# Kernel tuning notes

Measured on AMD Instinct MI355X. Metric: run time of the kernel, lower is better.

## Reference

```python
import jax, jax.numpy as jnp
import numpy as np

SNUM = 8           # number of select-PUF stages
PUF_LEN = 64       # arbiter PUF length -> phi dim = PUF_LEN + 1
BATCH = 262144     # number of challenge-response pairs
D = 2 ** SNUM      # 256 combinations


def _make_kron_tables():
    """Replicates the W/B kron construction from combineMPUF.__init__.
    Returns Wmat, Bmat of shape [SNUM, D]; row i is W[i]/B[i] (originally [1, D])."""
    tmpX = np.array([[1], [1]])
    Ws, Bs = [], []
    for i in range(SNUM):
        w = np.array([[-1], [1]])
        b = np.array([[1], [0]])
        for _ in range(i + 1, SNUM):
            w = np.kron(tmpX, w)
            b = np.kron(tmpX, b)
        for _ in range(i):
            w = np.kron(w, tmpX)
            b = np.kron(b, tmpX)
        Ws.append(w.T[0])
        Bs.append(b.T[0])
    return (jnp.asarray(np.stack(Ws), jnp.float32),
            jnp.asarray(np.stack(Bs), jnp.float32))


def setup_inputs() -> dict:
    key = jax.random.key(0)
    k_phi, k_ws, k_bs, k_wd, k_bd = jax.random.split(key, 5)
    F = PUF_LEN + 1
    scale = 1.0 / np.sqrt(F)  # ~ torch Linear init scale
    phi = jax.random.normal(k_phi, (BATCH, F), dtype=jnp.float32)
    W_S = jax.random.uniform(k_ws, (SNUM, F), jnp.float32, -scale, scale)
    b_S = jax.random.uniform(k_bs, (SNUM,), jnp.float32, -scale, scale)
    W_D = jax.random.uniform(k_wd, (D, F), jnp.float32, -scale, scale)
    b_D = jax.random.uniform(k_bd, (D,), jnp.float32, -scale, scale)
    Wmat, Bmat = _make_kron_tables()
    return {"phi": phi, "W_S": W_S, "b_S": b_S, "W_D": W_D, "b_D": b_D,
            "Wmat": Wmat, "Bmat": Bmat}


def reference(phi, W_S, b_S, W_D, b_D, Wmat, Bmat):
    # phi: [B, F]; W_S: [SNUM, F]; W_D: [D, F]; Wmat/Bmat: [SNUM, D]
    Sdelta = phi @ W_S.T + b_S            # [B, SNUM]
    Ddelta = phi @ W_D.T + b_D            # [B, D]
    Souts = jax.nn.sigmoid(Sdelta)        # [B, SNUM]
    Douts = jax.nn.sigmoid(Ddelta)        # [B, D]
    # sigmoid-gated outer-product chain: M = prod_i (s_i * w_i + b_i)
    M = jnp.ones_like(Douts)
    for i in range(SNUM):                 # small fixed structural loop
        M = M * (Souts[:, i:i + 1] * Wmat[i] + Bmat[i])
    ans = jnp.sum(Douts * M * 0.99999, axis=-1, keepdims=True)  # [B, 1]
    reliability_output = jnp.abs(Sdelta)  # [B, SNUM]
    return ans, reliability_output
```

## Files before the change

### kernel.cpp

```cpp
#include <hip/hip_runtime.h>

typedef float  f32x4  __attribute__((ext_vector_type(4)));
typedef float  f32x4a __attribute__((ext_vector_type(4), aligned(4)));
typedef __bf16 bf16x8 __attribute__((ext_vector_type(8)));
typedef short  short8 __attribute__((ext_vector_type(8)));

#define F      65
#define NTT    17
#define KS3    3
#define RPB    256
#define NCHUNK (NTT*KS3*64)
#define NEGL2E -1.4426950408889634f

__device__ __forceinline__ float fast_sigmoid(float x) {
  float e = __builtin_amdgcn_exp2f(NEGL2E * x);
  return __builtin_amdgcn_rcpf(1.0f + e);
}
__device__ __forceinline__ float sig_prescaled(float a) {
  return __builtin_amdgcn_rcpf(1.0f + __builtin_amdgcn_exp2f(a));
}
template<int CTRL>
__device__ __forceinline__ float dpp_mov(float v) {
  return __builtin_bit_cast(float,
    __builtin_amdgcn_update_dpp(0, __builtin_bit_cast(int, v), CTRL, 0xF, 0xF, true));
}
__device__ __forceinline__ float reduce16(float v) {
  v += dpp_mov<0xB1>(v);
  v += dpp_mov<0x4E>(v);
  v += dpp_mov<0x141>(v);
  v += dpp_mov<0x140>(v);
  return v;
}

__global__ void prep_w(const float* __restrict__ W_S, const float* __restrict__ b_S,
                       const float* __restrict__ W_D, const float* __restrict__ b_D,
                       unsigned short* __restrict__ wsb) {
  int b = blockIdx.x;
  int t = b / 3, s = b % 3;
  int l = threadIdx.x;
  int c = l & 15, q = l >> 4;
  short8 out;
#pragma unroll
  for (int j = 0; j < 8; ++j) {
    int k = 32 * s + 8 * q + j;
    float v = 0.0f;
    if (t < 16) {
      int n = 16 * t + c;
      if (k < F)       v = NEGL2E * W_D[n * F + k];
      else if (k == F) v = NEGL2E * b_D[n];
    } else if (c < 8) {
      if (k < F)       v = W_S[c * F + k];
      else if (k == F) v = b_S[c];
    }
    unsigned int u = __builtin_bit_cast(unsigned int, v);
    u += 0x7FFFu + ((u >> 16) & 1u);
    out[j] = (short)(u >> 16);
  }
  reinterpret_cast<short8*>(wsb)[b * 64 + l] = out;
}

__launch_bounds__(512, 4)
__global__ void mpuf_main(const float* __restrict__ phi,
                          const unsigned short* __restrict__ wsb,
                          float* __restrict__ out_ans,
                          float* __restrict__ out_rel) {
  __shared__ short8 ldsB[NCHUNK];
  __shared__ float  soutv[RPB][12];
  __shared__ float  mtT[16][260];

  const int tid  = threadIdx.x;
  const int wave = tid >> 6;
  const int l    = tid & 63;
  const int c    = l & 15;
  const int q    = l >> 4;
  const int wrow = wave * 32;
  const int R0b  = wrow + q * 4;
  const int brow = blockIdx.x * RPB;

  float* relbuf = &mtT[0][0];

  const float* prow0 = phi + (size_t)(brow + wrow + c) * F;
  const float* prow1 = prow0 + (size_t)16 * F;

  f32x4a f40[4], f41[4];
#pragma unroll
  for (int s = 0; s < 2; ++s) {
    f40[2 * s]     = *reinterpret_cast<const f32x4a*>(prow0 + 32 * s + 8 * q);
    f40[2 * s + 1] = *reinterpret_cast<const f32x4a*>(prow0 + 32 * s + 8 * q + 4);
    f41[2 * s]     = *reinterpret_cast<const f32x4a*>(prow1 + 32 * s + 8 * q);
    f41[2 * s + 1] = *reinterpret_cast<const f32x4a*>(prow1 + 32 * s + 8 * q + 4);
  }
  const float a640 = prow0[64];
  const float a641 = prow1[64];

  const short8* wsv = reinterpret_cast<const short8*>(wsb);
#pragma unroll
  for (int i = 0; i < 7; ++i) {
    int idx = tid + i * 512;
    if (idx < NCHUNK) ldsB[idx] = wsv[idx];
  }

  bf16x8 af0[3], af1[3];
#pragma unroll
  for (int s = 0; s < 2; ++s) {
    bf16x8 v0, v1;
#pragma unroll
    for (int j = 0; j < 4; ++j) {
      v0[j]     = (__bf16)f40[s * 2][j];
      v0[j + 4] = (__bf16)f40[s * 2 + 1][j];
      v1[j]     = (__bf16)f41[s * 2][j];
      v1[j + 4] = (__bf16)f41[s * 2 + 1][j];
    }
    af0[s] = v0; af1[s] = v1;
  }
  {
    bf16x8 v0 = {}, v1 = {};
    if (q == 0) {
      v0[0] = (__bf16)a640; v0[1] = (__bf16)1.0f;
      v1[0] = (__bf16)a641; v1[1] = (__bf16)1.0f;
    }
    af0[2] = v0; af1[2] = v1;
  }

  __syncthreads();

  f32x4 aS0 = {}, aS1 = {};
#pragma unroll
  for (int s = 0; s < KS3; ++s) {
    bf16x8 b = __builtin_bit_cast(bf16x8, ldsB[(16 * KS3 + s) * 64 + l]);
    aS0 = __builtin_amdgcn_mfma_f32_16x16x32_bf16(af0[s], b, aS0, 0, 0, 0);
    aS1 = __builtin_amdgcn_mfma_f32_16x16x32_bf16(af1[s], b, aS1, 0, 0, 0);
  }

  short8 bnxt[3];
#pragma unroll
  for (int s = 0; s < 3; ++s) bnxt[s] = ldsB[s * 64 + l];

  if (c < 8) {
#pragma unroll
    for (int r = 0; r < 4; ++r) {
      const int R0 = R0b + r, R1 = R0 + 16;
      relbuf[R0 * 8 + c] = fabsf(aS0[r]);
      relbuf[R1 * 8 + c] = fabsf(aS1[r]);
      soutv[R0][c] = fast_sigmoid(aS0[r]);
      soutv[R1][c] = fast_sigmoid(aS1[r]);
    }
  }

  {
    const int row = l >> 1, half = l & 1;
    f32x4 v = *reinterpret_cast<const f32x4*>(&relbuf[(wrow + row) * 8 + half * 4]);
    *reinterpret_cast<f32x4*>(
        &out_rel[(size_t)(brow + wrow + row) * 8 + half * 4]) = v;
  }

  __syncthreads();

  float Ml0[4], Ml1[4];
#pragma unroll
  for (int rr = 0; rr < 8; ++rr) {
    const int R = wrow + (rr & 4) * 4 + q * 4 + (rr & 3);
    f32x4 s03 = *reinterpret_cast<const f32x4*>(&soutv[R][0]);
    f32x4 s47 = *reinterpret_cast<const f32x4*>(&soutv[R][4]);
    float m = 0.99999f;
    m *= (c & 1) ? s03[0] : 1.0f - s03[0];
    m *= (c & 2) ? s03[1] : 1.0f - s03[1];
    m *= (c & 4) ? s03[2] : 1.0f - s03[2];
    m *= (c & 8) ? s03[3] : 1.0f - s03[3];
    if (rr < 4) Ml0[rr & 3] = m; else Ml1[rr & 3] = m;
    float mt = (c & 1) ? s47[0] : 1.0f - s47[0];
    mt *= (c & 2) ? s47[1] : 1.0f - s47[1];
    mt *= (c & 4) ? s47[2] : 1.0f - s47[2];
    mt *= (c & 8) ? s47[3] : 1.0f - s47[3];
    mtT[c][R] = mt;
  }

  float ans0[4] = {0, 0, 0, 0}, ans1[4] = {0, 0, 0, 0};

#pragma unroll 1
  for (int t = 0; t < 16; ++t) {
    short8 bt[3];
#pragma unroll
    for (int s = 0; s < 3; ++s) bt[s] = bnxt[s];
    const int tn = (t < 15) ? t + 1 : 15;
#pragma unroll
    for (int s = 0; s < 3; ++s)
      bnxt[s] = ldsB[(tn * KS3 + s) * 64 + l];
    f32x4 w0 = *reinterpret_cast<const f32x4*>(&mtT[t][R0b]);
    f32x4 w1 = *reinterpret_cast<const f32x4*>(&mtT[t][R0b + 16]);
    f32x4 A0 = {}, A1 = {};
#pragma unroll
    for (int s = 0; s < KS3; ++s) {
      bf16x8 b = __builtin_bit_cast(bf16x8, bt[s]);
      A0 = __builtin_amdgcn_mfma_f32_16x16x32_bf16(af0[s], b, A0, 0, 0, 0);
      A1 = __builtin_amdgcn_mfma_f32_16x16x32_bf16(af1[s], b, A1, 0, 0, 0);
    }
#pragma unroll
    for (int r = 0; r < 4; ++r) {
      ans0[r] = fmaf(sig_prescaled(A0[r]), w0[r], ans0[r]);
      ans1[r] = fmaf(sig_prescaled(A1[r]), w1[r], ans1[r]);
    }
  }

  f32x4 o0, o1;
#pragma unroll
  for (int r = 0; r < 4; ++r) {
    o0[r] = reduce16(Ml0[r] * ans0[r]);
    o1[r] = reduce16(Ml1[r] * ans1[r]);
  }
  if (c == 0) {
    *reinterpret_cast<f32x4*>(&out_ans[brow + wrow + q * 4])      = o0;
    *reinterpret_cast<f32x4*>(&out_ans[brow + wrow + 16 + q * 4]) = o1;
  }
}

extern "C" void kernel_launch(void* const* d_in, const int* in_sizes, int n_in,
                              void* d_out, int out_size, void* d_ws, size_t ws_size,
                              hipStream_t stream) {
  const float* phi = (const float*)d_in[0];
  const float* W_S = (const float*)d_in[1];
  const float* b_S = (const float*)d_in[2];
  const float* W_D = (const float*)d_in[3];
  const float* b_D = (const float*)d_in[4];
  const int rows = in_sizes[0] / F;
  unsigned short* wsb = (unsigned short*)d_ws;
  float* out_ans = (float*)d_out;
  float* out_rel = out_ans + rows;
  hipLaunchKernelGGL(prep_w, dim3(NTT * KS3), dim3(64), 0, stream,
                     W_S, b_S, W_D, b_D, wsb);
  hipLaunchKernelGGL(mpuf_main, dim3(rows / RPB), dim3(512), 0, stream,
                     phi, wsb, out_ans, out_rel);
}
```

Before: 36.92 us.

## Make main kernel persistent over two tiles with prefetch of next phi rows

```diff
diff --git a/kernel.cpp b/kernel.cpp
--- a/kernel.cpp
+++ b/kernel.cpp
@@ -10,6 +10,8 @@
 #define KS3    3
 #define RPB    256
 #define NCHUNK (NTT*KS3*64)
+#define GRID   512
+#define NITER  2
 #define NEGL2E -1.4426950408889634f
 
 __device__ __forceinline__ float fast_sigmoid(float x) {
@@ -75,13 +77,10 @@
   const int q    = l >> 4;
   const int wrow = wave * 32;
   const int R0b  = wrow + q * 4;
-  const int brow = blockIdx.x * RPB;
-
   float* relbuf = &mtT[0][0];
 
-  const float* prow0 = phi + (size_t)(brow + wrow + c) * F;
+  const float* prow0 = phi + (size_t)(blockIdx.x * RPB + wrow + c) * F;
   const float* prow1 = prow0 + (size_t)16 * F;
-
   f32x4a f40[4], f41[4];
 #pragma unroll
   for (int s = 0; s < 2; ++s) {
@@ -90,8 +89,8 @@
     f41[2 * s]     = *reinterpret_cast<const f32x4a*>(prow1 + 32 * s + 8 * q);
     f41[2 * s + 1] = *reinterpret_cast<const f32x4a*>(prow1 + 32 * s + 8 * q + 4);
   }
-  const float a640 = prow0[64];
-  const float a641 = prow1[64];
+  float a640 = prow0[64];
+  float a641 = prow1[64];
 
   const short8* wsv = reinterpret_cast<const short8*>(wsb);
 #pragma unroll
@@ -99,118 +98,138 @@
     int idx = tid + i * 512;
     if (idx < NCHUNK) ldsB[idx] = wsv[idx];
   }
-
-  bf16x8 af0[3], af1[3];
-#pragma unroll
-  for (int s = 0; s < 2; ++s) {
-    bf16x8 v0, v1;
-#pragma unroll
-    for (int j = 0; j < 4; ++j) {
-      v0[j]     = (__bf16)f40[s * 2][j];
-      v0[j + 4] = (__bf16)f40[s * 2 + 1][j];
-      v1[j]     = (__bf16)f41[s * 2][j];
-      v1[j + 4] = (__bf16)f41[s * 2 + 1][j];
-    }
-    af0[s] = v0; af1[s] = v1;
-  }
-  {
-    bf16x8 v0 = {}, v1 = {};
-    if (q == 0) {
-      v0[0] = (__bf16)a640; v0[1] = (__bf16)1.0f;
-      v1[0] = (__bf16)a641; v1[1] = (__bf16)1.0f;
-    }
-    af0[2] = v0; af1[2] = v1;
-  }
-
   __syncthreads();
 
-  f32x4 aS0 = {}, aS1 = {};
-#pragma unroll
-  for (int s = 0; s < KS3; ++s) {
-    bf16x8 b = __builtin_bit_cast(bf16x8, ldsB[(16 * KS3 + s) * 64 + l]);
-    aS0 = __builtin_amdgcn_mfma_f32_16x16x32_bf16(af0[s], b, aS0, 0, 0, 0);
-    aS1 = __builtin_amdgcn_mfma_f32_16x16x32_bf16(af1[s], b, aS1, 0, 0, 0);
-  }
-
-  short8 bnxt[3];
-#pragma unroll
-  for (int s = 0; s < 3; ++s) bnxt[s] = ldsB[s * 64 + l];
-
-  if (c < 8) {
+#pragma unroll 1
+  for (int it = 0; it < NITER; ++it) {
+    const int tl   = blockIdx.x + it * GRID;
+    const int brow = tl * RPB;
+    if (it) __syncthreads();
+
+    bf16x8 af0[3], af1[3];
+#pragma unroll
+    for (int s = 0; s < 2; ++s) {
+      bf16x8 v0, v1;
+#pragma unroll
+      for (int j = 0; j < 4; ++j) {
+        v0[j]     = (__bf16)f40[s * 2][j];
+        v0[j + 4] = (__bf16)f40[s * 2 + 1][j];
+        v1[j]     = (__bf16)f41[s * 2][j];
+        v1[j + 4] = (__bf16)f41[s * 2 + 1][j];
+      }
+      af0[s] = v0; af1[s] = v1;
+    }
+    {
+      bf16x8 v0 = {}, v1 = {};
+      if (q == 0) {
+        v0[0] = (__bf16)a640; v0[1] = (__bf16)1.0f;
+        v1[0] = (__bf16)a641; v1[1] = (__bf16)1.0f;
+      }
+      af0[2] = v0; af1[2] = v1;
+    }
+
+    if (it + 1 < NITER) {
+      const float* nrow0 = phi + (size_t)((tl + GRID) * RPB + wrow + c) * F;
+      const float* nrow1 = nrow0 + (size_t)16 * F;
+#pragma unroll
+      for (int s = 0; s < 2; ++s) {
+        f40[2 * s]     = *reinterpret_cast<const f32x4a*>(nrow0 + 32 * s + 8 * q);
+        f40[2 * s + 1] = *reinterpret_cast<const f32x4a*>(nrow0 + 32 * s + 8 * q + 4);
+        f41[2 * s]     = *reinterpret_cast<const f32x4a*>(nrow1 + 32 * s + 8 * q);
+        f41[2 * s + 1] = *reinterpret_cast<const f32x4a*>(nrow1 + 32 * s + 8 * q + 4);
+      }
+      a640 = nrow0[64];
+      a641 = nrow1[64];
+    }
+
+    f32x4 aS0 = {}, aS1 = {};
+#pragma unroll
+    for (int s = 0; s < KS3; ++s) {
+      bf16x8 b = __builtin_bit_cast(bf16x8, ldsB[(16 * KS3 + s) * 64 + l]);
+      aS0 = __builtin_amdgcn_mfma_f32_16x16x32_bf16(af0[s], b, aS0, 0, 0, 0);
+      aS1 = __builtin_amdgcn_mfma_f32_16x16x32_bf16(af1[s], b, aS1, 0, 0, 0);
+    }
+
+    short8 bnxt[3];
+#pragma unroll
+    for (int s = 0; s < 3; ++s) bnxt[s] = ldsB[s * 64 + l];
+
+    if (c < 8) {
+#pragma unroll
+      for (int r = 0; r < 4; ++r) {
+        const int R0 = R0b + r, R1 = R0 + 16;
+        relbuf[R0 * 8 + c] = fabsf(aS0[r]);
+        relbuf[R1 * 8 + c] = fabsf(aS1[r]);
+        soutv[R0][c] = fast_sigmoid(aS0[r]);
+        soutv[R1][c] = fast_sigmoid(aS1[r]);
+      }
+    }
+
+    {
+      const int row = l >> 1, half = l & 1;
+      f32x4 v = *reinterpret_cast<const f32x4*>(&relbuf[(wrow + row) * 8 + half * 4]);
+      *reinterpret_cast<f32x4*>(
+          &out_rel[(size_t)(brow + wrow + row) * 8 + half * 4]) = v;
+    }
+
+    __syncthreads();
+
+    float Ml0[4], Ml1[4];
+#pragma unroll
+    for (int rr = 0; rr < 8; ++rr) {
+      const int R = wrow + (rr & 4) * 4 + q * 4 + (rr & 3);
+      f32x4 s03 = *reinterpret_cast<const f32x4*>(&soutv[R][0]);
+      f32x4 s47 = *reinterpret_cast<const f32x4*>(&soutv[R][4]);
+      float m = 0.99999f;
+      m *= (c & 1) ? s03[0] : 1.0f - s03[0];
+      m *= (c & 2) ? s03[1] : 1.0f - s03[1];
+      m *= (c & 4) ? s03[2] : 1.0f - s03[2];
+      m *= (c & 8) ? s03[3] : 1.0f - s03[3];
+      if (rr < 4) Ml0[rr & 3] = m; else Ml1[rr & 3] = m;
+      float mt = (c & 1) ? s47[0] : 1.0f - s47[0];
+      mt *= (c & 2) ? s47[1] : 1.0f - s47[1];
+      mt *= (c & 4) ? s47[2] : 1.0f - s47[2];
+      mt *= (c & 8) ? s47[3] : 1.0f - s47[3];
+      mtT[c][R] = mt;
+    }
+
+    float ans0[4] = {0, 0, 0, 0}, ans1[4] = {0, 0, 0, 0};
+
+#pragma unroll 1
+    for (int t = 0; t < 16; ++t) {
+      short8 bt[3];
+#pragma unroll
+      for (int s = 0; s < 3; ++s) bt[s] = bnxt[s];
+      const int tn = (t < 15) ? t + 1 : 15;
+#pragma unroll
+      for (int s = 0; s < 3; ++s)
+        bnxt[s] = ldsB[(tn * KS3 + s) * 64 + l];
+      f32x4 w0 = *reinterpret_cast<const f32x4*>(&mtT[t][R0b]);
+      f32x4 w1 = *reinterpret_cast<const f32x4*>(&mtT[t][R0b + 16]);
+      f32x4 A0 = {}, A1 = {};
+#pragma unroll
+      for (int s = 0; s < KS3; ++s) {
+        bf16x8 b = __builtin_bit_cast(bf16x8, bt[s]);
+        A0 = __builtin_amdgcn_mfma_f32_16x16x32_bf16(af0[s], b, A0, 0, 0, 0);
+        A1 = __builtin_amdgcn_mfma_f32_16x16x32_bf16(af1[s], b, A1, 0, 0, 0);
+      }
+#pragma unroll
+      for (int r = 0; r < 4; ++r) {
+        ans0[r] = fmaf(sig_prescaled(A0[r]), w0[r], ans0[r]);
+        ans1[r] = fmaf(sig_prescaled(A1[r]), w1[r], ans1[r]);
+      }
+    }
+
+    f32x4 o0, o1;
 #pragma unroll
     for (int r = 0; r < 4; ++r) {
-      const int R0 = R0b + r, R1 = R0 + 16;
-      relbuf[R0 * 8 + c] = fabsf(aS0[r]);
-      relbuf[R1 * 8 + c] = fabsf(aS1[r]);
-      soutv[R0][c] = fast_sigmoid(aS0[r]);
-      soutv[R1][c] = fast_sigmoid(aS1[r]);
-    }
-  }
-
-  {
-    const int row = l >> 1, half = l & 1;
-    f32x4 v = *reinterpret_cast<const f32x4*>(&relbuf[(wrow + row) * 8 + half * 4]);
-    *reinterpret_cast<f32x4*>(
-        &out_rel[(size_t)(brow + wrow + row) * 8 + half * 4]) = v;
-  }
-
-  __syncthreads();
-
-  float Ml0[4], Ml1[4];
-#pragma unroll
-  for (int rr = 0; rr < 8; ++rr) {
-    const int R = wrow + (rr & 4) * 4 + q * 4 + (rr & 3);
-    f32x4 s03 = *reinterpret_cast<const f32x4*>(&soutv[R][0]);
-    f32x4 s47 = *reinterpret_cast<const f32x4*>(&soutv[R][4]);
-    float m = 0.99999f;
-    m *= (c & 1) ? s03[0] : 1.0f - s03[0];
-    m *= (c & 2) ? s03[1] : 1.0f - s03[1];
-    m *= (c & 4) ? s03[2] : 1.0f - s03[2];
-    m *= (c & 8) ? s03[3] : 1.0f - s03[3];
-    if (rr < 4) Ml0[rr & 3] = m; else Ml1[rr & 3] = m;
-    float mt = (c & 1) ? s47[0] : 1.0f - s47[0];
-    mt *= (c & 2) ? s47[1] : 1.0f - s47[1];
-    mt *= (c & 4) ? s47[2] : 1.0f - s47[2];
-    mt *= (c & 8) ? s47[3] : 1.0f - s47[3];
-    mtT[c][R] = mt;
-  }
-
-  float ans0[4] = {0, 0, 0, 0}, ans1[4] = {0, 0, 0, 0};
-
-#pragma unroll 1
-  for (int t = 0; t < 16; ++t) {
-    short8 bt[3];
-#pragma unroll
-    for (int s = 0; s < 3; ++s) bt[s] = bnxt[s];
-    const int tn = (t < 15) ? t + 1 : 15;
-#pragma unroll
-    for (int s = 0; s < 3; ++s)
-      bnxt[s] = ldsB[(tn * KS3 + s) * 64 + l];
-    f32x4 w0 = *reinterpret_cast<const f32x4*>(&mtT[t][R0b]);
-    f32x4 w1 = *reinterpret_cast<const f32x4*>(&mtT[t][R0b + 16]);
-    f32x4 A0 = {}, A1 = {};
-#pragma unroll
-    for (int s = 0; s < KS3; ++s) {
-      bf16x8 b = __builtin_bit_cast(bf16x8, bt[s]);
-      A0 = __builtin_amdgcn_mfma_f32_16x16x32_bf16(af0[s], b, A0, 0, 0, 0);
-      A1 = __builtin_amdgcn_mfma_f32_16x16x32_bf16(af1[s], b, A1, 0, 0, 0);
-    }
-#pragma unroll
-    for (int r = 0; r < 4; ++r) {
-      ans0[r] = fmaf(sig_prescaled(A0[r]), w0[r], ans0[r]);
-      ans1[r] = fmaf(sig_prescaled(A1[r]), w1[r], ans1[r]);
-    }
-  }
-
-  f32x4 o0, o1;
-#pragma unroll
-  for (int r = 0; r < 4; ++r) {
-    o0[r] = reduce16(Ml0[r] * ans0[r]);
-    o1[r] = reduce16(Ml1[r] * ans1[r]);
-  }
-  if (c == 0) {
-    *reinterpret_cast<f32x4*>(&out_ans[brow + wrow + q * 4])      = o0;
-    *reinterpret_cast<f32x4*>(&out_ans[brow + wrow + 16 + q * 4]) = o1;
+      o0[r] = reduce16(Ml0[r] * ans0[r]);
+      o1[r] = reduce16(Ml1[r] * ans1[r]);
+    }
+    if (c == 0) {
+      *reinterpret_cast<f32x4*>(&out_ans[brow + wrow + q * 4])      = o0;
+      *reinterpret_cast<f32x4*>(&out_ans[brow + wrow + 16 + q * 4]) = o1;
+    }
   }
 }
 
@@ -223,11 +242,12 @@
   const float* W_D = (const float*)d_in[3];
   const float* b_D = (const float*)d_in[4];
   const int rows = in_sizes[0] / F;
+  (void)rows;
   unsigned short* wsb = (unsigned short*)d_ws;
   float* out_ans = (float*)d_out;
   float* out_rel = out_ans + rows;
   hipLaunchKernelGGL(prep_w, dim3(NTT * KS3), dim3(64), 0, stream,
                      W_S, b_S, W_D, b_D, wsb);
-  hipLaunchKernelGGL(mpuf_main, dim3(rows / RPB), dim3(512), 0, stream,
+  hipLaunchKernelGGL(mpuf_main, dim3(GRID), dim3(512), 0, stream,
                      phi, wsb, out_ans, out_rel);
 }
```

Measured after the change: 54.72 us. 1.48x slower.
